# Kernel optimization log

Measured on AMD Instinct MI355X. Metric: run time of the kernel, lower is better.

The kernel has to match this reference:

```python
import jax, jax.numpy as jnp
import numpy as np

B, T, E = 8, 2048, 1024
H = 16
HD = E // H            # per-head hidden_dim = 64
DFF = 4 * E
DC = T // 512          # decay_constant = 4
EPS = 1e-5


def setup_inputs() -> dict:
    key = jax.random.key(0)
    ks = jax.random.split(key, 8)
    return {
        "x": jax.random.normal(ks[0], (B, T, E), jnp.float32),
        # per-head input projections (Linear(dim, hidden_dim) x H)
        "w_proj": jax.random.normal(ks[1], (H, E, HD), jnp.float32) / np.sqrt(E),
        "b_proj": jnp.zeros((H, HD), jnp.float32),
        # causal mixing weights: first H//2 heads are Col-repeat, last H//2 Row-repeat
        "mix_w": jax.random.normal(ks[2], (H, T), jnp.float32),
        "mix_b": jnp.zeros((H, T), jnp.float32),
        "decay": jnp.ones((H,), jnp.float32),   # decay_value params (init ones as in torch)
        "out_w": jax.random.normal(ks[3], (E, E), jnp.float32) / np.sqrt(E),
        "out_b": jnp.zeros((E,), jnp.float32),
        "ln1_g": jnp.ones((E,), jnp.float32),
        "ln1_b": jnp.zeros((E,), jnp.float32),
        "ln2_g": jnp.ones((E,), jnp.float32),
        "ln2_b": jnp.zeros((E,), jnp.float32),
        "ff_w1": jax.random.normal(ks[4], (E, DFF), jnp.float32) / np.sqrt(E),
        "ff_b1": jnp.zeros((DFF,), jnp.float32),
        "ff_w2": jax.random.normal(ks[5], (DFF, E), jnp.float32) / np.sqrt(DFF),
        "ff_b2": jnp.zeros((E,), jnp.float32),
        "index": 0,
    }


def _layernorm(x, g, b):
    mu = jnp.mean(x, -1, keepdims=True)
    var = jnp.var(x, -1, keepdims=True)
    return (x - mu) * jax.lax.rsqrt(var + EPS) * g + b


def _mix_matrices(mix_w, decay):
    # Col heads: M[i,j] = v[j] * d**((j-i)/DC) for j>=i else 0
    # Row heads: M[i,j] = v[i] * d**((j-i)/DC) for j>=i else 0
    i = jnp.arange(T)[:, None]
    j = jnp.arange(T)[None, :]
    d = jnp.clip(decay, 0.9, 1.0)                                   # (H,)
    expo = (j - i).astype(jnp.float32) / DC                         # (T,T)
    dec = d[:, None, None] ** expo                                  # (H,T,T)
    causal = (j >= i)
    half = H // 2
    Mcol = jnp.where(causal, mix_w[:half, None, :] * dec[:half], 0.0)
    Mrow = jnp.where(causal, mix_w[half:, :, None] * dec[half:], 0.0)
    return jnp.concatenate([Mcol, Mrow], axis=0)                    # (H,T,T)


def reference(x, w_proj, b_proj, mix_w, mix_b, decay, out_w, out_b,
              ln1_g, ln1_b, ln2_g, ln2_b, ff_w1, ff_b1, ff_w2, ff_b2, index):
    # ---- token-mixing sub-block (parallel path of MixedRepeatHeads) ----
    res = x
    h = _layernorm(x, ln1_g, ln1_b)
    # per-head projection: (B,T,E) x (H,E,HD) -> (B,H,T,HD)
    p = jnp.einsum('bte,hef->bhtf', h, w_proj) + b_proj[:, None, :]
    M = _mix_matrices(mix_w, decay)
    # causal decay mixing along time: out[b,h,s,f] = sum_t p[b,h,t,f] * M[h,t,s]
    mixed = jnp.einsum('bhtf,hts->bhsf', p, M) + mix_b[None, :, :, None]
    # concat heads along feature dim -> (B,T,E)
    mixed = mixed.transpose(0, 2, 1, 3).reshape(B, T, E)
    mixed = mixed @ out_w + out_b
    x = mixed + res
    # ---- feed-forward sub-block ----
    res = x
    h = _layernorm(x, ln2_g, ln2_b)
    h = jax.nn.gelu(h @ ff_w1 + ff_b1) @ ff_w2 + ff_b2
    return h + res
```

## Files before the change

kernel.cpp:

```cpp
#include <hip/hip_runtime.h>


#define TT 2048
#define EE 1024
#define HHD 64
#define MROWS 16384
#define SC_L 64

typedef __bf16 bf16x8 __attribute__((ext_vector_type(8)));
typedef float f32x4 __attribute__((ext_vector_type(4)));
typedef unsigned short u16;
typedef unsigned int u32;

__device__ __forceinline__ u16 f2bf(float f) {
  u32 u = __builtin_bit_cast(u32, f);
  u += 0x7FFFu + ((u >> 16) & 1u);
  return (u16)(u >> 16);
}
__device__ __forceinline__ float bf2f(u16 s) {
  u32 u = ((u32)s) << 16;
  return __builtin_bit_cast(float, u);
}
__device__ __forceinline__ float gelu_f(float x) {
  float x2 = x * x;
  float e = -1.5957691216057308f * x * __builtin_fmaf(0.044715f, x2, 1.0f);
  return x * __builtin_amdgcn_rcpf(1.0f + __expf(e));
}
__device__ __forceinline__ void gload_lds16(const void* g, void* l) {
  __builtin_amdgcn_global_load_lds(
      (const __attribute__((address_space(1))) u32*)g,
      (__attribute__((address_space(3))) u32*)l, 16, 0, 0);
}
__device__ __forceinline__ void wg_barrier() {
  asm volatile("" ::: "memory");
  __builtin_amdgcn_s_barrier();
  asm volatile("" ::: "memory");
}

__global__ __launch_bounds__(256) void transpose_to_bf16(
    const float* __restrict__ src, u16* __restrict__ dst, int R, int C,
    long sbs, long dbs) {
  __shared__ float tile[32][33];
  src += (long)blockIdx.z * sbs;
  dst += (long)blockIdx.z * dbs;
  int c0 = blockIdx.x * 32, r0 = blockIdx.y * 32;
  int tx = threadIdx.x, ty = threadIdx.y;
#pragma unroll
  for (int i = 0; i < 4; i++)
    tile[ty + i * 8][tx] = src[(long)(r0 + ty + i * 8) * C + c0 + tx];
  __syncthreads();
#pragma unroll
  for (int i = 0; i < 4; i++)
    dst[(long)(c0 + ty + i * 8) * R + r0 + tx] = f2bf(tile[tx][ty + i * 8]);
}

__global__ __launch_bounds__(256) void ln_to_bf16(
    const float* __restrict__ x, const float* __restrict__ gam,
    const float* __restrict__ bet, u16* __restrict__ y) {
  int row = blockIdx.x;
  int tid = threadIdx.x;
  float4 v = ((const float4*)x)[row * 256 + tid];
  float s = v.x + v.y + v.z + v.w;
  float s2 = v.x * v.x + v.y * v.y + v.z * v.z + v.w * v.w;
#pragma unroll
  for (int off = 1; off < 64; off <<= 1) {
    s += __shfl_xor(s, off);
    s2 += __shfl_xor(s2, off);
  }
  __shared__ float red[8];
  int w = tid >> 6;
  if ((tid & 63) == 0) { red[w] = s; red[4 + w] = s2; }
  __syncthreads();
  s = red[0] + red[1] + red[2] + red[3];
  s2 = red[4] + red[5] + red[6] + red[7];
  float mu = s * (1.0f / 1024.0f);
  float var = s2 * (1.0f / 1024.0f) - mu * mu;
  float rstd = rsqrtf(var + 1e-5f);
  int e0 = tid * 4;
  ushort4 o;
  o.x = f2bf((v.x - mu) * rstd * gam[e0 + 0] + bet[e0 + 0]);
  o.y = f2bf((v.y - mu) * rstd * gam[e0 + 1] + bet[e0 + 1]);
  o.z = f2bf((v.z - mu) * rstd * gam[e0 + 2] + bet[e0 + 2]);
  o.w = f2bf((v.w - mu) * rstd * gam[e0 + 3] + bet[e0 + 3]);
  ((ushort4*)y)[row * 256 + tid] = o;
}

template <int EPI>
__global__ __launch_bounds__(1024) void gemm256w16(
    const u16* __restrict__ A, const u16* __restrict__ Bt,
    const float* __restrict__ bias, const float* __restrict__ res, void* outp,
    int M, int N, int K, int px, int gxp, int byper) {
  __shared__ u16 lds[65536];
  const int tid = threadIdx.x;
  const int w = tid >> 6, lane = tid & 63;
  const int wm = w >> 2, wn = w & 3;
  const int l15 = lane & 15, lk = lane >> 4;

  const int gx = (int)gridDim.x;
  const int bid = (int)blockIdx.y * gx + (int)blockIdx.x;
  const int xcd = bid & 7, i = bid >> 3;
  const int bx = (xcd % gxp) * px + (i % px);
  const int by = (xcd / gxp) * byper + (i / px);
  const int m0 = by * 256, n0 = bx * 256;

  const int srow = w * 8 + (lane >> 3);
  const int sslot = (lane & 7) ^ (lane >> 3);
  const u16* aS = A + (size_t)(m0 + srow) * K + sslot * 8;
  const u16* bS = Bt + (size_t)(n0 + srow) * K + sslot * 8;

  f32x4 acc[4][4];
  const f32x4 z = {0.f, 0.f, 0.f, 0.f};
#pragma unroll
  for (int mi = 0; mi < 4; mi++)
#pragma unroll
    for (int ni = 0; ni < 4; ni++) acc[mi][ni] = z;

  const int sl0 = (lk ^ (l15 & 7)) * 8;
  const int sl1 = ((4 + lk) ^ (l15 & 7)) * 8;

#define STAGE_ALL(C, KT) { \
    u16* lb = lds + (C) * 32768 + w * 512; \
    gload_lds16(aS + (KT), lb); \
    gload_lds16(aS + (size_t)128 * K + (KT), lb + 8192); \
    gload_lds16(bS + (KT), lb + 16384); \
    gload_lds16(bS + (size_t)128 * K + (KT), lb + 24576); }

  const int nt = K >> 6;
  STAGE_ALL(0, 0);

  for (int t = 0; t < nt; ++t) {
    const int cur = t & 1, nx = cur ^ 1;
    if (t + 1 < nt) {
      STAGE_ALL(nx, (t + 1) << 6);
      asm volatile("s_waitcnt vmcnt(4)" ::: "memory");
    } else {
      asm volatile("s_waitcnt vmcnt(0)" ::: "memory");
    }
    wg_barrier();

    const u16* lA = lds + cur * 32768 + (wm * 64 + l15) * 64;
    const u16* lB = lds + cur * 32768 + 16384 + (wn * 64 + l15) * 64;
#pragma unroll
    for (int ks = 0; ks < 2; ks++) {
      const int sl = ks ? sl1 : sl0;
      bf16x8 bq[4];
#pragma unroll
      for (int ni = 0; ni < 4; ni++)
        bq[ni] = *(const bf16x8*)(lB + ni * 1024 + sl);
      __builtin_amdgcn_s_setprio(1);
#pragma unroll
      for (int mi = 0; mi < 4; mi++) {
        bf16x8 af = *(const bf16x8*)(lA + mi * 1024 + sl);
#pragma unroll
        for (int ni = 0; ni < 4; ni++)
          acc[mi][ni] = __builtin_amdgcn_mfma_f32_16x16x32_bf16(af, bq[ni],
                                                                acc[mi][ni], 0, 0, 0);
      }
      __builtin_amdgcn_s_setprio(0);
    }
    wg_barrier();
  }
#undef STAGE_ALL

#pragma unroll
  for (int mi = 0; mi < 4; mi++) {
#pragma unroll
    for (int ni = 0; ni < 4; ni++) {
      int n = n0 + wn * 64 + ni * 16 + l15;
      float bvv = bias[n];
#pragma unroll
      for (int r = 0; r < 4; r++) {
        int m = m0 + wm * 64 + mi * 16 + lk * 4 + r;
        size_t idx = (size_t)m * N + n;
        float v = acc[mi][ni][r] + bvv;
        if (EPI == 0) {
          ((u16*)outp)[idx] = f2bf(v);
        } else if (EPI == 1) {
          ((float*)outp)[idx] = v + res[idx];
        } else {
          ((u16*)outp)[idx] = f2bf(gelu_f(v));
        }
      }
    }
  }
}

__global__ __launch_bounds__(64) void scan_carry(
    const u16* __restrict__ p, const float* __restrict__ mix_w,
    const float* __restrict__ decay, float* __restrict__ carry) {
  int blk = blockIdx.x;
  int c = blk & 31, h = (blk >> 5) & 15, b = blk >> 9;
  int f = threadIdx.x;
  float d = fminf(fmaxf(decay[h], 0.9f), 1.0f);
  float r = powf(d, 0.25f);
  size_t base = ((size_t)b * TT + c * SC_L) * EE + h * HHD + f;
  const float* mw = mix_w + h * TT + c * SC_L;
  bool isRow = (h >= 8);
  float S = 0.f;
#pragma unroll 4
  for (int t = 0; t < SC_L; t++) {
    float pv = bf2f(p[base + (size_t)t * EE]);
    float q = isRow ? mw[t] * pv : pv;
    S = r * S + q;
  }
  carry[blk * 64 + f] = S;
}

__global__ __launch_bounds__(64) void scan_apply(
    const u16* __restrict__ p, const float* __restrict__ mix_w,
    const float* __restrict__ mix_b, const float* __restrict__ decay,
    const float* __restrict__ carry, u16* __restrict__ mixed) {
  int blk = blockIdx.x;
  int c = blk & 31, h = (blk >> 5) & 15, b = blk >> 9;
  int f = threadIdx.x;
  float d = fminf(fmaxf(decay[h], 0.9f), 1.0f);
  float r = powf(d, 0.25f);
  float rl = powf(r, (float)SC_L);
  int cb = blk - c;
  float S = 0.f;
  for (int cc = 0; cc < c; cc++) S = rl * S + carry[(cb + cc) * 64 + f];
  size_t base = ((size_t)b * TT + c * SC_L) * EE + h * HHD + f;
  const float* mw = mix_w + h * TT + c * SC_L;
  const float* mb = mix_b + h * TT + c * SC_L;
  bool isRow = (h >= 8);
  for (int t = 0; t < SC_L; t++) {
    float pv = bf2f(p[base + (size_t)t * EE]);
    float q = isRow ? mw[t] * pv : pv;
    S = r * S + q;
    float val = (isRow ? S : mw[t] * S) + mb[t];
    mixed[base + (size_t)t * EE] = f2bf(val);
  }
}

extern "C" void kernel_launch(void* const* d_in, const int* in_sizes, int n_in,
                              void* d_out, int out_size, void* d_ws, size_t ws_size,
                              hipStream_t stream) {
  const float* x = (const float*)d_in[0];
  const float* w_proj = (const float*)d_in[1];
  const float* b_proj = (const float*)d_in[2];
  const float* mix_w = (const float*)d_in[3];
  const float* mix_b = (const float*)d_in[4];
  const float* decay = (const float*)d_in[5];
  const float* out_w = (const float*)d_in[6];
  const float* out_b = (const float*)d_in[7];
  const float* ln1_g = (const float*)d_in[8];
  const float* ln1_b = (const float*)d_in[9];
  const float* ln2_g = (const float*)d_in[10];
  const float* ln2_b = (const float*)d_in[11];
  const float* ff_w1 = (const float*)d_in[12];
  const float* ff_b1 = (const float*)d_in[13];
  const float* ff_w2 = (const float*)d_in[14];
  const float* ff_b2 = (const float*)d_in[15];
  float* out = (float*)d_out;

  char* ws = (char*)d_ws;
  const size_t MiB = 1ull << 20;
  u16* wWp = (u16*)(ws + 0 * MiB);
  u16* wWo = (u16*)(ws + 2 * MiB);
  u16* wW1 = (u16*)(ws + 4 * MiB);
  u16* wW2 = (u16*)(ws + 12 * MiB);
  u16* wMix = (u16*)(ws + 20 * MiB);
  u16* wH = (u16*)(ws + 52 * MiB);
  u16* wP = (u16*)(ws + 84 * MiB);
  u16* wU = (u16*)(ws + 52 * MiB);
  float* wCarry = (float*)(ws + 180 * MiB);

  dim3 tb(32, 8);
  transpose_to_bf16<<<dim3(2, 32, 16), tb, 0, stream>>>(w_proj, wWp, 1024, 64,
                                                        65536L, 65536L);
  transpose_to_bf16<<<dim3(32, 32, 1), tb, 0, stream>>>(out_w, wWo, 1024, 1024, 0L, 0L);
  transpose_to_bf16<<<dim3(128, 32, 1), tb, 0, stream>>>(ff_w1, wW1, 1024, 4096, 0L, 0L);
  transpose_to_bf16<<<dim3(32, 128, 1), tb, 0, stream>>>(ff_w2, wW2, 4096, 1024, 0L, 0L);

  ln_to_bf16<<<dim3(MROWS), dim3(256), 0, stream>>>(x, ln1_g, ln1_b, wH);

  gemm256w16<0><<<dim3(4, 64), dim3(1024), 0, stream>>>(
      wH, wWp, b_proj, (const float*)nullptr, (void*)wP, MROWS, 1024, 1024,
      4, 1, 8);

  scan_carry<<<dim3(4096), dim3(64), 0, stream>>>(wP, mix_w, decay, wCarry);
  scan_apply<<<dim3(4096), dim3(64), 0, stream>>>(wP, mix_w, mix_b, decay, wCarry, wMix);

  gemm256w16<1><<<dim3(4, 64), dim3(1024), 0, stream>>>(
      wMix, wWo, out_b, x, (void*)out, MROWS, 1024, 1024,
      4, 1, 8);

  ln_to_bf16<<<dim3(MROWS), dim3(256), 0, stream>>>(out, ln2_g, ln2_b, wMix);

  gemm256w16<2><<<dim3(16, 64), dim3(1024), 0, stream>>>(
      wMix, wW1, ff_b1, (const float*)nullptr, (void*)wU, MROWS, 4096, 1024,
      4, 4, 32);

  gemm256w16<1><<<dim3(4, 64), dim3(1024), 0, stream>>>(
      wU, wW2, ff_b2, out, (void*)out, MROWS, 1024, 4096,
      2, 2, 16);
}
```

Measured before the change: 524.0 us.

## Restructure GEMM into 8-wave 4-stage pipeline and vectorize decay scan

The GEMM drops from 16 to 8 waves, so each wave now computes a 128x64 tile with twice as many accumulators. K steps shrink to 32, and loads run through a 4-buffer LDS ring with prefetch distance 2, which removes the second barrier per iteration and keeps more loads in flight. The scan kernels now give each thread 8 contiguous features, using 16-byte bf16 loads and stores and packing 8 chunks per block. This cuts per-element memory transactions and block count. In exchange the GEMM uses more registers per wave at lower occupancy, and the scan launches fewer threads.

```diff
diff --git a/kernel.cpp b/kernel.cpp
--- a/kernel.cpp
+++ b/kernel.cpp
@@ -11,6 +11,7 @@
 typedef float f32x4 __attribute__((ext_vector_type(4)));
 typedef unsigned short u16;
 typedef unsigned int u32;
+typedef u16 u16x8 __attribute__((ext_vector_type(8)));
 
 __device__ __forceinline__ u16 f2bf(float f) {
   u32 u = __builtin_bit_cast(u32, f);
@@ -86,7 +87,7 @@
 }
 
 template <int EPI>
-__global__ __launch_bounds__(1024) void gemm256w16(
+__global__ __launch_bounds__(512, 1) void gemm256q(
     const u16* __restrict__ A, const u16* __restrict__ Bt,
     const float* __restrict__ bias, const float* __restrict__ res, void* outp,
     int M, int N, int K, int px, int gxp, int byper) {
@@ -103,74 +104,78 @@
   const int by = (xcd / gxp) * byper + (i / px);
   const int m0 = by * 256, n0 = bx * 256;
 
-  const int srow = w * 8 + (lane >> 3);
-  const int sslot = (lane & 7) ^ (lane >> 3);
-  const u16* aS = A + (size_t)(m0 + srow) * K + sslot * 8;
-  const u16* bS = Bt + (size_t)(n0 + srow) * K + sslot * 8;
-
-  f32x4 acc[4][4];
+  const int srow = w * 16 + (lane >> 2);
+  const int gslot = (lane & 3) ^ ((srow >> 1) & 3);
+  const u16* aS = A + (size_t)(m0 + srow) * K + gslot * 8;
+  const u16* aS2 = A + (size_t)(m0 + 128 + srow) * K +
+                   (((lane & 3) ^ (((128 + srow) >> 1) & 3)) * 8);
+  const u16* bS = Bt + (size_t)(n0 + srow) * K + gslot * 8;
+  const u16* bS2 = Bt + (size_t)(n0 + 128 + srow) * K +
+                   (((lane & 3) ^ (((128 + srow) >> 1) & 3)) * 8);
+
+  f32x4 acc[8][4];
   const f32x4 z = {0.f, 0.f, 0.f, 0.f};
 #pragma unroll
-  for (int mi = 0; mi < 4; mi++)
+  for (int mi = 0; mi < 8; mi++)
 #pragma unroll
     for (int ni = 0; ni < 4; ni++) acc[mi][ni] = z;
 
-  const int sl0 = (lk ^ (l15 & 7)) * 8;
-  const int sl1 = ((4 + lk) ^ (l15 & 7)) * 8;
-
-#define STAGE_ALL(C, KT) { \
-    u16* lb = lds + (C) * 32768 + w * 512; \
-    gload_lds16(aS + (KT), lb); \
-    gload_lds16(aS + (size_t)128 * K + (KT), lb + 8192); \
-    gload_lds16(bS + (KT), lb + 16384); \
-    gload_lds16(bS + (size_t)128 * K + (KT), lb + 24576); }
-
-  const int nt = K >> 6;
-  STAGE_ALL(0, 0);
+  const int sl = (lk ^ ((l15 >> 1) & 3)) * 8;
+
+#define STAGE(BUF, T_) { \
+    u16* lb = lds + (BUF) * 16384 + w * 512; \
+    const int kt = (T_) << 5; \
+    gload_lds16(aS + kt, lb); \
+    gload_lds16(aS2 + kt, lb + 4096); \
+    gload_lds16(bS + kt, lb + 8192); \
+    gload_lds16(bS2 + kt, lb + 12288); }
+
+  const int nt = K >> 5;
+  STAGE(0, 0);
+  STAGE(1, 1);
 
   for (int t = 0; t < nt; ++t) {
-    const int cur = t & 1, nx = cur ^ 1;
-    if (t + 1 < nt) {
-      STAGE_ALL(nx, (t + 1) << 6);
+    if (t + 2 < nt) {
+      STAGE((t + 2) & 3, t + 2);
+      asm volatile("s_waitcnt vmcnt(8)" ::: "memory");
+    } else if (t + 1 < nt) {
       asm volatile("s_waitcnt vmcnt(4)" ::: "memory");
     } else {
       asm volatile("s_waitcnt vmcnt(0)" ::: "memory");
     }
     wg_barrier();
 
-    const u16* lA = lds + cur * 32768 + (wm * 64 + l15) * 64;
-    const u16* lB = lds + cur * 32768 + 16384 + (wn * 64 + l15) * 64;
-#pragma unroll
-    for (int ks = 0; ks < 2; ks++) {
-      const int sl = ks ? sl1 : sl0;
-      bf16x8 bq[4];
+    const u16* lA = lds + (t & 3) * 16384;
+    const u16* lB = lA + 8192;
+    bf16x8 bq[4];
+    {
+      const u16* bp = lB + (wn * 64 + l15) * 32 + sl;
+#pragma unroll
+      for (int ni = 0; ni < 4; ni++) bq[ni] = *(const bf16x8*)(bp + ni * 512);
+    }
+    const u16* ap = lA + (wm * 128 + l15) * 32 + sl;
+    __builtin_amdgcn_s_setprio(1);
+#pragma unroll
+    for (int mi = 0; mi < 8; mi++) {
+      bf16x8 af = *(const bf16x8*)(ap + mi * 512);
 #pragma unroll
       for (int ni = 0; ni < 4; ni++)
-        bq[ni] = *(const bf16x8*)(lB + ni * 1024 + sl);
-      __builtin_amdgcn_s_setprio(1);
-#pragma unroll
-      for (int mi = 0; mi < 4; mi++) {
-        bf16x8 af = *(const bf16x8*)(lA + mi * 1024 + sl);
-#pragma unroll
-        for (int ni = 0; ni < 4; ni++)
-          acc[mi][ni] = __builtin_amdgcn_mfma_f32_16x16x32_bf16(af, bq[ni],
-                                                                acc[mi][ni], 0, 0, 0);
-      }
-      __builtin_amdgcn_s_setprio(0);
-    }
-    wg_barrier();
-  }
-#undef STAGE_ALL
-
-#pragma unroll
-  for (int mi = 0; mi < 4; mi++) {
+        acc[mi][ni] = __builtin_amdgcn_mfma_f32_16x16x32_bf16(af, bq[ni],
+                                                              acc[mi][ni], 0, 0, 0);
+    }
+    __builtin_amdgcn_s_setprio(0);
+  }
+#undef STAGE
+
+#pragma unroll
+  for (int mi = 0; mi < 8; mi++) {
 #pragma unroll
     for (int ni = 0; ni < 4; ni++) {
       int n = n0 + wn * 64 + ni * 16 + l15;
       float bvv = bias[n];
 #pragma unroll
       for (int r = 0; r < 4; r++) {
-        int m = m0 + wm * 64 + mi * 16 + lk * 4 + r;
+        int m = m0 + wm * 128 + mi * 16 + lk * 4 + r;
         size_t idx = (size_t)m * N + n;
         float v = acc[mi][ni][r] + bvv;
         if (EPI == 0) {
@@ -188,47 +193,62 @@
 __global__ __launch_bounds__(64) void scan_carry(
     const u16* __restrict__ p, const float* __restrict__ mix_w,
     const float* __restrict__ decay, float* __restrict__ carry) {
-  int blk = blockIdx.x;
-  int c = blk & 31, h = (blk >> 5) & 15, b = blk >> 9;
-  int f = threadIdx.x;
+  int chunk = blockIdx.x * 8 + (threadIdx.x >> 3);
+  int fg = threadIdx.x & 7;
+  int c = chunk & 31, h = (chunk >> 5) & 15, b = chunk >> 9;
   float d = fminf(fmaxf(decay[h], 0.9f), 1.0f);
   float r = powf(d, 0.25f);
-  size_t base = ((size_t)b * TT + c * SC_L) * EE + h * HHD + f;
+  size_t base = (((size_t)b * TT + c * SC_L) * EE + h * HHD + fg * 8) >> 3;
+  const u16x8* p8 = (const u16x8*)p;
   const float* mw = mix_w + h * TT + c * SC_L;
   bool isRow = (h >= 8);
-  float S = 0.f;
-#pragma unroll 4
+  float S[8] = {0.f, 0.f, 0.f, 0.f, 0.f, 0.f, 0.f, 0.f};
   for (int t = 0; t < SC_L; t++) {
-    float pv = bf2f(p[base + (size_t)t * EE]);
-    float q = isRow ? mw[t] * pv : pv;
-    S = r * S + q;
-  }
-  carry[blk * 64 + f] = S;
+    u16x8 v = p8[base + (size_t)t * (EE / 8)];
+    float wv = isRow ? mw[t] : 1.0f;
+#pragma unroll
+    for (int j = 0; j < 8; j++) S[j] = r * S[j] + wv * bf2f(v[j]);
+  }
+  float* cp = carry + chunk * 64 + fg * 8;
+#pragma unroll
+  for (int j = 0; j < 8; j++) cp[j] = S[j];
 }
 
 __global__ __launch_bounds__(64) void scan_apply(
     const u16* __restrict__ p, const float* __restrict__ mix_w,
     const float* __restrict__ mix_b, const float* __restrict__ decay,
     const float* __restrict__ carry, u16* __restrict__ mixed) {
-  int blk = blockIdx.x;
-  int c = blk & 31, h = (blk >> 5) & 15, b = blk >> 9;
-  int f = threadIdx.x;
+  int chunk = blockIdx.x * 8 + (threadIdx.x >> 3);
+  int fg = threadIdx.x & 7;
+  int c = chunk & 31, h = (chunk >> 5) & 15, b = chunk >> 9;
   float d = fminf(fmaxf(decay[h], 0.9f), 1.0f);
   float r = powf(d, 0.25f);
   float rl = powf(r, (float)SC_L);
-  int cb = blk - c;
-  float S = 0.f;
-  for (int cc = 0; cc < c; cc++) S = rl * S + carry[(cb + cc) * 64 + f];
-  size_t base = ((size_t)b * TT + c * SC_L) * EE + h * HHD + f;
+  int cb = chunk - c;
+  float S[8] = {0.f, 0.f, 0.f, 0.f, 0.f, 0.f, 0.f, 0.f};
+  for (int cc = 0; cc < c; cc++) {
+    const float* cp = carry + (cb + cc) * 64 + fg * 8;
+#pragma unroll
+    for (int j = 0; j < 8; j++) S[j] = rl * S[j] + cp[j];
+  }
+  size_t base = (((size_t)b * TT + c * SC_L) * EE + h * HHD + fg * 8) >> 3;
+  const u16x8* p8 = (const u16x8*)p;
+  u16x8* m8 = (u16x8*)mixed;
   const float* mw = mix_w + h * TT + c * SC_L;
   const float* mb = mix_b + h * TT + c * SC_L;
   bool isRow = (h >= 8);
   for (int t = 0; t < SC_L; t++) {
-    float pv = bf2f(p[base + (size_t)t * EE]);
-    float q = isRow ? mw[t] * pv : pv;
-    S = r * S + q;
-    float val = (isRow ? S : mw[t] * S) + mb[t];
-    mixed[base + (size_t)t * EE] = f2bf(val);
+    u16x8 v = p8[base + (size_t)t * (EE / 8)];
+    float wq = isRow ? mw[t] : 1.0f;
+    float wo = isRow ? 1.0f : mw[t];
+    float bb = mb[t];
+    u16x8 o;
+#pragma unroll
+    for (int j = 0; j < 8; j++) {
+      S[j] = r * S[j] + wq * bf2f(v[j]);
+      o[j] = f2bf(wo * S[j] + bb);
+    }
+    m8[base + (size_t)t * (EE / 8)] = o;
   }
 }
 
@@ -274,24 +294,24 @@
 
   ln_to_bf16<<<dim3(MROWS), dim3(256), 0, stream>>>(x, ln1_g, ln1_b, wH);
 
-  gemm256w16<0><<<dim3(4, 64), dim3(1024), 0, stream>>>(
+  gemm256q<0><<<dim3(4, 64), dim3(512), 0, stream>>>(
       wH, wWp, b_proj, (const float*)nullptr, (void*)wP, MROWS, 1024, 1024,
       4, 1, 8);
 
-  scan_carry<<<dim3(4096), dim3(64), 0, stream>>>(wP, mix_w, decay, wCarry);
-  scan_apply<<<dim3(4096), dim3(64), 0, stream>>>(wP, mix_w, mix_b, decay, wCarry, wMix);
-
-  gemm256w16<1><<<dim3(4, 64), dim3(1024), 0, stream>>>(
+  scan_carry<<<dim3(512), dim3(64), 0, stream>>>(wP, mix_w, decay, wCarry);
+  scan_apply<<<dim3(512), dim3(64), 0, stream>>>(wP, mix_w, mix_b, decay, wCarry, wMix);
+
+  gemm256q<1><<<dim3(4, 64), dim3(512), 0, stream>>>(
       wMix, wWo, out_b, x, (void*)out, MROWS, 1024, 1024,
       4, 1, 8);
 
   ln_to_bf16<<<dim3(MROWS), dim3(256), 0, stream>>>(out, ln2_g, ln2_b, wMix);
 
-  gemm256w16<2><<<dim3(16, 64), dim3(1024), 0, stream>>>(
+  gemm256q<2><<<dim3(16, 64), dim3(512), 0, stream>>>(
       wMix, wW1, ff_b1, (const float*)nullptr, (void*)wU, MROWS, 4096, 1024,
       4, 4, 32);
 
-  gemm256w16<1><<<dim3(4, 64), dim3(1024), 0, stream>>>(
+  gemm256q<1><<<dim3(4, 64), dim3(512), 0, stream>>>(
       wU, wW2, ff_b2, out, (void*)out, MROWS, 1024, 4096,
       2, 2, 16);
 }
```

Measured after the change: 520.4 us. About the same (-0.7%).
